# Kernel tuning notes

Hardware: AMD Instinct MI355X
Metric: run time of the kernel (lower is better)

Reference implementation:

```python
import jax, jax.numpy as jnp
import numpy as np

D_MODEL = 16   # output feature dim of channel_proj
D_STATE = 8
D_CONV = 2
D_INNER = 4    # expand * inner mamba d_model (2*2)
DT_RANK = 1    # ceil(2/16)
NUM_PAIRS = 36
B, W, T = 8, 8, 1024


def setup_inputs() -> dict:
    key = jax.random.key(0)
    ks = jax.random.split(key, 12)
    s = 0.5
    return {
        "raw_signals": jax.random.normal(ks[0], (B, W, NUM_PAIRS, 2, T), jnp.float32),
        "in_proj_w": jax.random.normal(ks[1], (2 * D_INNER, 2), jnp.float32) * s,
        "conv_w": jax.random.normal(ks[2], (D_INNER, D_CONV), jnp.float32) * s,
        "conv_b": jax.random.normal(ks[3], (D_INNER,), jnp.float32) * 0.1,
        "x_proj_w": jax.random.normal(ks[4], (DT_RANK + 2 * D_STATE, D_INNER), jnp.float32) * s,
        "dt_proj_w": jax.random.normal(ks[5], (D_INNER, DT_RANK), jnp.float32) * s,
        "dt_proj_b": jax.random.normal(ks[6], (D_INNER,), jnp.float32) * 0.1,
        # S4D-real init: A_log = log(arange(1..d_state)) per inner channel
        "A_log": jnp.log(jnp.broadcast_to(jnp.arange(1, D_STATE + 1, dtype=jnp.float32), (D_INNER, D_STATE))),
        "D_skip": jnp.ones((D_INNER,), jnp.float32),
        "out_proj_w": jax.random.normal(ks[7], (2, D_INNER), jnp.float32) * s,
        "proj_w": jax.random.normal(ks[8], (D_MODEL, 2), jnp.float32) * s,
        "proj_b": jax.random.normal(ks[9], (D_MODEL,), jnp.float32) * 0.1,
    }


def _mamba_forward(x_in, in_proj_w, conv_w, conv_b, x_proj_w, dt_proj_w,
                   dt_proj_b, A_log, D_skip, out_proj_w):
    # x_in: (N, T, 2)
    N, Tlen, _ = x_in.shape
    xz = jnp.einsum('ntc,dc->ntd', x_in, in_proj_w)          # (N,T,2*d_inner)
    x, z = jnp.split(xz, 2, axis=-1)                          # (N,T,d_inner) each
    # causal depthwise conv1d, kernel size D_CONV
    xp = jnp.pad(x, ((0, 0), (D_CONV - 1, 0), (0, 0)))
    x = sum(xp[:, k:k + Tlen] * conv_w[:, k] for k in range(D_CONV)) + conv_b
    x = jax.nn.silu(x)
    # input-dependent dt, B, C
    x_dbl = jnp.einsum('ntd,ed->nte', x, x_proj_w)            # (N,T,dt_rank+2*d_state)
    dt, Bm, Cm = jnp.split(x_dbl, [DT_RANK, DT_RANK + D_STATE], axis=-1)
    dt = jax.nn.softplus(jnp.einsum('ntr,dr->ntd', dt, dt_proj_w) + dt_proj_b)
    A = -jnp.exp(A_log)                                       # (d_inner,d_state)
    deltaA = jnp.exp(dt[..., None] * A)                       # (N,T,d_inner,d_state)
    deltaBx = dt[..., None] * Bm[:, :, None, :] * x[..., None]

    def step(h, inputs):
        dA_t, dBx_t, c_t = inputs
        h = dA_t * h + dBx_t                                  # (N,d_inner,d_state)
        y_t = jnp.einsum('nds,ns->nd', h, c_t)
        return h, y_t

    h0 = jnp.zeros((N, D_INNER, D_STATE), x.dtype)
    _, ys = jax.lax.scan(
        step, h0,
        (deltaA.transpose(1, 0, 2, 3), deltaBx.transpose(1, 0, 2, 3), Cm.transpose(1, 0, 2)))
    y = ys.transpose(1, 0, 2) + x * D_skip                    # (N,T,d_inner)
    y = y * jax.nn.silu(z)
    return jnp.einsum('ntd,cd->ntc', y, out_proj_w)           # (N,T,2)


def reference(raw_signals, in_proj_w, conv_w, conv_b, x_proj_w, dt_proj_w,
              dt_proj_b, A_log, D_skip, out_proj_w, proj_w, proj_b):
    Bsz, Wn, P, C, Tlen = raw_signals.shape
    # per-window loop in torch does identical math -> flatten windows into batch
    x_in = raw_signals.transpose(0, 1, 2, 4, 3).reshape(-1, Tlen, C)  # (B*W*P, T, 2)
    out = _mamba_forward(x_in, in_proj_w, conv_w, conv_b, x_proj_w, dt_proj_w,
                         dt_proj_b, A_log, D_skip, out_proj_w)
    feat = out.mean(axis=1)                                   # (B*W*P, 2)
    proj = jax.nn.relu(feat @ proj_w.T + proj_b)              # dropout is eval no-op
    proj = proj.reshape(Bsz, Wn, P, -1)                       # (B,W,P,d_model)
    return proj.mean(axis=2)                                  # (B,W,d_model)
```

## Files before the change

kernel.cpp:

```cpp
#include <hip/hip_runtime.h>
#include <hip/hip_fp16.h>


typedef float v2f __attribute__((ext_vector_type(2)));

#define TT 1024
#define TC 32
#define GSEG 4
#define SEGLEN (TT / GSEG)
#define NCHUNK (SEGLEN / TC)
#define NUM_PAIRS 36
#define NSEQ 2304

#define DT_OFF 0
#define DS_OFF 128
#define BC_OFF 256
#define BC_STRIDE 33
#define PER_HALF_STRIDE 528
#define PER_WAVE (2 * PER_HALF_STRIDE)
#define STAGE_TOTAL (GSEG * PER_WAVE)

__device__ __forceinline__ float fast_silu(float v) {
    float e = __builtin_amdgcn_exp2f(v * -1.4426950408889634f);
    return v * __builtin_amdgcn_rcpf(1.0f + e);
}
__device__ __forceinline__ float fast_softplus(float v) {
    float e = __builtin_amdgcn_exp2f(v * 1.4426950408889634f);
    return __builtin_amdgcn_logf(1.0f + e) * 0.6931471805599453f;
}
__device__ __forceinline__ uint pk_h2(float a, float b) {
    return __builtin_bit_cast(uint, __builtin_amdgcn_cvt_pkrtz(a, b));
}

__global__ __launch_bounds__(256, 6)
void pm_kernel(const float* __restrict__ raw,
               const float* __restrict__ in_proj_w,
               const float* __restrict__ conv_w,
               const float* __restrict__ conv_b,
               const float* __restrict__ x_proj_w,
               const float* __restrict__ dt_proj_w,
               const float* __restrict__ dt_proj_b,
               const float* __restrict__ A_log,
               const float* __restrict__ D_skip,
               const float* __restrict__ out_proj_w,
               const float* __restrict__ proj_w,
               const float* __restrict__ proj_b,
               float* __restrict__ out)
{
    __shared__ float lds[STAGE_TOTAL];

    const int tid  = threadIdx.x;
    const int wid  = tid >> 6;
    const int lane = tid & 63;
    const int half = lane >> 5;
    const int lh   = lane & 31;
    const int n    = blockIdx.x * 2 + half;
    const float* rp = raw + (size_t)n * (2 * TT);

    float* hb = lds + wid * PER_WAVE + half * PER_HALF_STRIDE;

    float ip0[8], ip1[8];
#pragma unroll
    for (int j = 0; j < 8; ++j) { ip0[j] = in_proj_w[2*j]; ip1[j] = in_proj_w[2*j+1]; }
    float cw0[4], cw1[4], cbv[4], dpw[4], dpb[4], Dsk[4], ow0[4], ow1[4], xp0[4];
#pragma unroll
    for (int d = 0; d < 4; ++d) {
        cw0[d] = conv_w[2*d]; cw1[d] = conv_w[2*d+1]; cbv[d] = conv_b[d];
        dpw[d] = dt_proj_w[d]; dpb[d] = dt_proj_b[d];
        Dsk[d] = D_skip[d]; ow0[d] = out_proj_w[d]; ow1[d] = out_proj_w[4+d];
        xp0[d] = x_proj_w[d];
    }
    v2f xbc[8][4];
#pragma unroll
    for (int s = 0; s < 8; ++s)
#pragma unroll
        for (int d = 0; d < 4; ++d)
            xbc[s][d] = (v2f){x_proj_w[4*(1+s) + d], x_proj_w[4*(9+s) + d]};

    const float LOG2E = 1.4426950408889634f;
    const int   d_idx = lh >> 3;
    const int   s_idx = lh & 7;
    const float A2ds  = -__expf(A_log[lh]) * LOG2E;
    const float owd0  = out_proj_w[d_idx];
    const float owd1  = out_proj_w[4 + d_idx];

    const float* dtp = hb + DT_OFF + d_idx;
    const uint*  dsp = (const uint*)(hb + DS_OFF) + d_idx;
    const uint*  bcp = (const uint*)(hb + BC_OFF) + s_idx * BC_STRIDE;

    float A_run = 1.0f, hB = 0.0f, W = 0.0f, S = 0.0f;
    float sacc0 = 0.f, sacc1 = 0.f;

    const int seg0 = wid * SEGLEN;

    int t0 = seg0 + lh;
    float c0  = rp[t0];
    float c1  = rp[TT + t0];
    float c0m = (t0 > 0) ? rp[t0 - 1]      : 0.0f;
    float c1m = (t0 > 0) ? rp[TT + t0 - 1] : 0.0f;

    for (int chunk = 0; chunk < NCHUNK; ++chunk) {
        float p0 = 0.f, p1 = 0.f, p0m = 0.f, p1m = 0.f;
        if (chunk + 1 < NCHUNK) {
            int tn = seg0 + (chunk + 1) * TC + lh;
            p0  = rp[tn];       p1  = rp[TT + tn];
            p0m = rp[tn - 1];   p1m = rp[TT + tn - 1];
        }

        float x[4], sz[4];
#pragma unroll
        for (int d = 0; d < 4; ++d) {
            float xz  = ip0[d]*c0  + ip1[d]*c1;
            float xm1 = ip0[d]*c0m + ip1[d]*c1m;
            float zv  = ip0[4+d]*c0 + ip1[4+d]*c1;
            float v   = xm1*cw0[d] + xz*cw1[d] + cbv[d];
            x[d]  = fast_silu(v);
            sz[d] = fast_silu(zv);
        }

        float dtin = xp0[0]*x[0] + xp0[1]*x[1] + xp0[2]*x[2] + xp0[3]*x[3];

        v2f bc[8];
#pragma unroll
        for (int s = 0; s < 8; ++s) {
            v2f a = xbc[s][0] * (v2f){x[0], x[0]};
            a = __builtin_elementwise_fma(xbc[s][1], (v2f){x[1], x[1]}, a);
            a = __builtin_elementwise_fma(xbc[s][2], (v2f){x[2], x[2]}, a);
            bc[s] = __builtin_elementwise_fma(xbc[s][3], (v2f){x[3], x[3]}, a);
        }

        float dt[4];
#pragma unroll
        for (int d = 0; d < 4; ++d) {
            dt[d] = fast_softplus(dtin*dpw[d] + dpb[d]);
            float g = x[d] * Dsk[d] * sz[d];
            sacc0 = fmaf(g, ow0[d], sacc0);
            sacc1 = fmaf(g, ow1[d], sacc1);
        }

        *(float4*)(hb + DT_OFF + lh*4) = make_float4(dt[0], dt[1], dt[2], dt[3]);
        *(uint4*)((uint*)(hb + DS_OFF) + lh*4) =
            make_uint4(pk_h2(dt[0]*x[0], sz[0]), pk_h2(dt[1]*x[1], sz[1]),
                       pk_h2(dt[2]*x[2], sz[2]), pk_h2(dt[3]*x[3], sz[3]));
        uint* bcw = (uint*)(hb + BC_OFF) + lh;
#pragma unroll
        for (int s = 0; s < 8; ++s)
            bcw[s * BC_STRIDE] = pk_h2(bc[s].x, bc[s].y);

#pragma unroll
        for (int t2 = 0; t2 < TC; ++t2) {
            float dtv = dtp[t2*4];
            uint  uds = dsp[t2*4];
            uint  ubc = bcp[t2];
            __half2 prod = __hmul2(__builtin_bit_cast(__half2, uds),
                                   __builtin_bit_cast(__half2, ubc));
            float b = __half2float(__low2half(prod));
            float q = __half2float(__high2half(prod));
            float a = __builtin_amdgcn_exp2f(dtv * A2ds);
            A_run *= a;
            hB = fmaf(a, hB, b);
            W  = fmaf(A_run, q, W);
            S  = fmaf(hB, q, S);
        }

        c0 = p0; c1 = p1; c0m = p0m; c1m = p1m;
    }

    __syncthreads();
    float2* comb = (float2*)lds;
    comb[(half*GSEG + wid)*32 + lh] = make_float2(A_run, hB);
    __syncthreads();

    float h_in = 0.0f;
#pragma unroll
    for (int g = 0; g < GSEG; ++g) {
        if (g < wid) {
            float2 abg = comb[(half*GSEG + g)*32 + lh];
            h_in = fmaf(abg.x, h_in, abg.y);
        }
    }

    float F = fmaf(h_in, W, S);
    float tot0 = fmaf(F, owd0, sacc0);
    float tot1 = fmaf(F, owd1, sacc1);
#pragma unroll
    for (int m = 16; m >= 1; m >>= 1) {
        tot0 += __shfl_xor(tot0, m, 64);
        tot1 += __shfl_xor(tot1, m, 64);
    }
    float* part = lds + 1024;
    if (lh == 0) {
        part[(half*GSEG + wid)*2]     = tot0;
        part[(half*GSEG + wid)*2 + 1] = tot1;
    }
    __syncthreads();

    if (wid == 0 && lh < 16) {
        float f0 = 0.f, f1 = 0.f;
#pragma unroll
        for (int g = 0; g < GSEG; ++g) {
            f0 += part[(half*GSEG + g)*2];
            f1 += part[(half*GSEG + g)*2 + 1];
        }
        f0 *= (1.0f / (float)TT);
        f1 *= (1.0f / (float)TT);
        float pv = f0*proj_w[2*lh] + f1*proj_w[2*lh + 1] + proj_b[lh];
        pv = fmaxf(pv, 0.0f);
        atomicAdd(out + (n / NUM_PAIRS) * 16 + lh, pv * (1.0f / NUM_PAIRS));
    }
}

extern "C" void kernel_launch(void* const* d_in, const int* in_sizes, int n_in,
                              void* d_out, int out_size, void* d_ws, size_t ws_size,
                              hipStream_t stream)
{
    const float* raw        = (const float*)d_in[0];
    const float* in_proj_w  = (const float*)d_in[1];
    const float* conv_w     = (const float*)d_in[2];
    const float* conv_b     = (const float*)d_in[3];
    const float* x_proj_w   = (const float*)d_in[4];
    const float* dt_proj_w  = (const float*)d_in[5];
    const float* dt_proj_b  = (const float*)d_in[6];
    const float* A_log      = (const float*)d_in[7];
    const float* D_skip     = (const float*)d_in[8];
    const float* out_proj_w = (const float*)d_in[9];
    const float* proj_w     = (const float*)d_in[10];
    const float* proj_b     = (const float*)d_in[11];

    hipMemsetAsync(d_out, 0, (size_t)out_size * sizeof(float), stream);

    pm_kernel<<<dim3(NSEQ / 2), dim3(256), 0, stream>>>(
        raw, in_proj_w, conv_w, conv_b, x_proj_w, dt_proj_w, dt_proj_b,
        A_log, D_skip, out_proj_w, proj_w, proj_b, (float*)d_out);
}
```

Baseline: 130.3 us.

## Split each sequence into eight time segments across one block

Each block now handles a single sequence, with all eight half-waves scanning separate 128-step segments, where before each block handled two sequences with four segments each. The grid doubles to one block per sequence. The serial scan length per thread halves, which shortens the dependency chain but adds a longer cross-segment combine and more blocks, each paying the setup and final-reduction overhead. Launch bounds occupancy hint is lowered from 6 to 4.

```diff
diff --git a/kernel.cpp b/kernel.cpp
--- a/kernel.cpp
+++ b/kernel.cpp
@@ -6,8 +6,8 @@
 
 #define TT 1024
 #define TC 32
-#define GSEG 4
-#define SEGLEN (TT / GSEG)
+#define NSEGS 8
+#define SEGLEN (TT / NSEGS)
 #define NCHUNK (SEGLEN / TC)
 #define NUM_PAIRS 36
 #define NSEQ 2304
@@ -18,7 +18,7 @@
 #define BC_STRIDE 33
 #define PER_HALF_STRIDE 528
 #define PER_WAVE (2 * PER_HALF_STRIDE)
-#define STAGE_TOTAL (GSEG * PER_WAVE)
+#define STAGE_TOTAL (4 * PER_WAVE)
 
 __device__ __forceinline__ float fast_silu(float v) {
     float e = __builtin_amdgcn_exp2f(v * -1.4426950408889634f);
@@ -32,7 +32,7 @@
     return __builtin_bit_cast(uint, __builtin_amdgcn_cvt_pkrtz(a, b));
 }
 
-__global__ __launch_bounds__(256, 6)
+__global__ __launch_bounds__(256, 4)
 void pm_kernel(const float* __restrict__ raw,
                const float* __restrict__ in_proj_w,
                const float* __restrict__ conv_w,
@@ -54,7 +54,8 @@
     const int lane = tid & 63;
     const int half = lane >> 5;
     const int lh   = lane & 31;
-    const int n    = blockIdx.x * 2 + half;
+    const int g    = wid * 2 + half;
+    const int n    = blockIdx.x;
     const float* rp = raw + (size_t)n * (2 * TT);
 
     float* hb = lds + wid * PER_WAVE + half * PER_HALF_STRIDE;
@@ -91,7 +92,7 @@
     float A_run = 1.0f, hB = 0.0f, W = 0.0f, S = 0.0f;
     float sacc0 = 0.f, sacc1 = 0.f;
 
-    const int seg0 = wid * SEGLEN;
+    const int seg0 = g * SEGLEN;
 
     int t0 = seg0 + lh;
     float c0  = rp[t0];
@@ -133,9 +134,9 @@
 #pragma unroll
         for (int d = 0; d < 4; ++d) {
             dt[d] = fast_softplus(dtin*dpw[d] + dpb[d]);
-            float g = x[d] * Dsk[d] * sz[d];
-            sacc0 = fmaf(g, ow0[d], sacc0);
-            sacc1 = fmaf(g, ow1[d], sacc1);
+            float g2 = x[d] * Dsk[d] * sz[d];
+            sacc0 = fmaf(g2, ow0[d], sacc0);
+            sacc1 = fmaf(g2, ow1[d], sacc1);
         }
 
         *(float4*)(hb + DT_OFF + lh*4) = make_float4(dt[0], dt[1], dt[2], dt[3]);
@@ -168,14 +169,14 @@
 
     __syncthreads();
     float2* comb = (float2*)lds;
-    comb[(half*GSEG + wid)*32 + lh] = make_float2(A_run, hB);
+    comb[g*32 + lh] = make_float2(A_run, hB);
     __syncthreads();
 
     float h_in = 0.0f;
 #pragma unroll
-    for (int g = 0; g < GSEG; ++g) {
-        if (g < wid) {
-            float2 abg = comb[(half*GSEG + g)*32 + lh];
+    for (int gg = 0; gg < NSEGS - 1; ++gg) {
+        if (gg < g) {
+            float2 abg = comb[gg*32 + lh];
             h_in = fmaf(abg.x, h_in, abg.y);
         }
     }
@@ -188,25 +189,25 @@
         tot0 += __shfl_xor(tot0, m, 64);
         tot1 += __shfl_xor(tot1, m, 64);
     }
-    float* part = lds + 1024;
+    float* part = lds + 512;
     if (lh == 0) {
-        part[(half*GSEG + wid)*2]     = tot0;
-        part[(half*GSEG + wid)*2 + 1] = tot1;
+        part[g*2]     = tot0;
+        part[g*2 + 1] = tot1;
     }
     __syncthreads();
 
-    if (wid == 0 && lh < 16) {
+    if (tid < 16) {
         float f0 = 0.f, f1 = 0.f;
 #pragma unroll
-        for (int g = 0; g < GSEG; ++g) {
-            f0 += part[(half*GSEG + g)*2];
-            f1 += part[(half*GSEG + g)*2 + 1];
+        for (int gg = 0; gg < NSEGS; ++gg) {
+            f0 += part[gg*2];
+            f1 += part[gg*2 + 1];
         }
         f0 *= (1.0f / (float)TT);
         f1 *= (1.0f / (float)TT);
-        float pv = f0*proj_w[2*lh] + f1*proj_w[2*lh + 1] + proj_b[lh];
+        float pv = f0*proj_w[2*tid] + f1*proj_w[2*tid + 1] + proj_b[tid];
         pv = fmaxf(pv, 0.0f);
-        atomicAdd(out + (n / NUM_PAIRS) * 16 + lh, pv * (1.0f / NUM_PAIRS));
+        atomicAdd(out + (n / NUM_PAIRS) * 16 + tid, pv * (1.0f / NUM_PAIRS));
     }
 }
 
@@ -229,7 +230,7 @@
 
     hipMemsetAsync(d_out, 0, (size_t)out_size * sizeof(float), stream);
 
-    pm_kernel<<<dim3(NSEQ / 2), dim3(256), 0, stream>>>(
+    pm_kernel<<<dim3(NSEQ), dim3(256), 0, stream>>>(
         raw, in_proj_w, conv_w, conv_b, x_proj_w, dt_proj_w, dt_proj_b,
         A_log, D_skip, out_proj_w, proj_w, proj_b, (float*)d_out);
 }
```

Result: faster. 116.3 us (-10.7%).
